# Kernel optimization log

Hardware: AMD Instinct MI355X
Metric: run time of the kernel (lower is better)

The kernel has to match this reference:

```python
import jax, jax.numpy as jnp
import numpy as np

N_NODES = 50000
N_EDGES = 500000
NFEAT = 128
NHID = 128
NOUT = 16


def setup_inputs() -> dict:
    key = jax.random.key(0)
    ks = jax.random.split(key, 8)
    x = jax.random.normal(ks[0], (N_NODES, NFEAT), dtype=jnp.float32)
    edge_src = jax.random.randint(ks[1], (N_EDGES,), 0, N_NODES, dtype=jnp.int32)
    edge_dst = jax.random.randint(ks[2], (N_EDGES,), 0, N_NODES, dtype=jnp.int32)
    edge_weight = jax.random.uniform(ks[3], (N_EDGES,), dtype=jnp.float32)
    # Glorot-ish init for linear weights, zero bias (PyG GCNConv default bias=0)
    def glorot(k, fan_in, fan_out):
        s = jnp.sqrt(6.0 / (fan_in + fan_out))
        return jax.random.uniform(k, (fan_in, fan_out), jnp.float32, -s, s)
    W1 = glorot(ks[4], NFEAT, NHID)
    W2 = glorot(ks[5], NHID, NHID)
    W3 = glorot(ks[6], NHID, NOUT)
    b1 = jnp.zeros((NHID,), jnp.float32)
    b2 = jnp.zeros((NHID,), jnp.float32)
    b3 = jnp.zeros((NOUT,), jnp.float32)
    return {"x": x, "edge_src": edge_src, "edge_dst": edge_dst,
            "edge_weight": edge_weight, "W1": W1, "b1": b1,
            "W2": W2, "b2": b2, "W3": W3, "b3": b3}


def gcn_conv(x, src, dst, ew, W, b):
    """PyG GCNConv: symmetric-normalized aggregation with self-loops (weight 1).

    out_i = sum_{(j->i)} d_i^{-1/2} w_ji d_j^{-1/2} (x_j W) + d_i^{-1} (x_i W) + b
    where d_i = 1 + sum of incoming edge weights.
    """
    n = x.shape[0]
    xw = x @ W                                            # [N, F_out]
    deg = jax.ops.segment_sum(ew, dst, num_segments=n) + 1.0  # self-loop weight 1
    dinv = jnp.where(deg > 0, jax.lax.rsqrt(deg), 0.0)    # d^{-1/2}
    norm = dinv[src] * ew * dinv[dst]                     # [E]
    agg = jax.ops.segment_sum(xw[src] * norm[:, None], dst, num_segments=n)
    self_loop = xw * (dinv * dinv)[:, None]               # d_i^{-1} * x_i W
    return agg + self_loop + b


def reference(x, edge_src, edge_dst, edge_weight, W1, b1, W2, b2, W3, b3):
    # Dropout layers are identity in eval mode.
    h = gcn_conv(x, edge_src, edge_dst, edge_weight, W1, b1)
    h = jax.nn.relu(h)
    h = gcn_conv(h, edge_src, edge_dst, edge_weight, W2, b2)
    h = jax.nn.relu(h)
    h = gcn_conv(h, edge_src, edge_dst, edge_weight, W3, b3)
    return jax.nn.log_softmax(h, axis=1)
```

## Files before the change

### kernel.cpp

```cpp
#include <hip/hip_runtime.h>
#include <math.h>

#define NN 50000
#define NE 500000
#define NF 128
#define NO 16
#define SCAN_B 1024
#define NPART 16
#define EBL 1954

static_assert(NN < 65536, "src must fit u16");

typedef _Float16 f16x8 __attribute__((ext_vector_type(8)));
typedef _Float16 f16x4 __attribute__((ext_vector_type(4)));
typedef float f32x4 __attribute__((ext_vector_type(4)));

union HU { unsigned short u; _Float16 h; };

__device__ inline float rec_w(unsigned int rec) {
    HU cu; cu.u = (unsigned short)(rec >> 16);
    return (float)cu.h;
}


__global__ void k_count_rank(const int* __restrict__ dst, int* __restrict__ pcnt,
                             int* __restrict__ rank, int E,
                             const float* __restrict__ W1, const float* __restrict__ W2,
                             _Float16* __restrict__ W1T, _Float16* __restrict__ W2T) {
    int b = blockIdx.x;
    if (b < EBL) {
        int part = b & (NPART - 1);
        int e = b * 256 + threadIdx.x;
        if (e < E) {
            int d = dst[e];
            rank[e] = atomicAdd(&pcnt[part * NN + d], 1);
        }
    } else {
        int idx = (b - EBL) * 256 + threadIdx.x;
        int r = idx >> 7, c = idx & 127;
        W1T[(size_t)c * NF + r] = (_Float16)W1[idx];
        W2T[(size_t)c * NF + r] = (_Float16)W2[idx];
    }
}

__global__ void k_scan1f(int* __restrict__ pcnt, int* __restrict__ offs_p,
                         int* __restrict__ bsums, int N) {
    __shared__ int sm[SCAN_B];
    int t = threadIdx.x;
    int i = blockIdx.x * SCAN_B + t;
    int c = 0;
    if (i < N) {
        int run = 0;
#pragma unroll
        for (int p = 0; p < NPART; ++p) {
            int v = pcnt[p * NN + i];
            pcnt[p * NN + i] = run;
            run += v;
        }
        c = run;
    }
    sm[t] = c;
    __syncthreads();
    for (int off = 1; off < SCAN_B; off <<= 1) {
        int x = (t >= off) ? sm[t - off] : 0;
        __syncthreads();
        sm[t] += x;
        __syncthreads();
    }
    if (i < N) offs_p[i] = sm[t] - c;
    if (t == SCAN_B - 1) bsums[blockIdx.x] = sm[t];
}

__global__ void k_scan2(int* __restrict__ bsums, int NB) {
    int t = threadIdx.x;
    int v = (t < NB) ? bsums[t] : 0;
    int orig = v;
#pragma unroll
    for (int off = 1; off < 64; off <<= 1) {
        int u = __shfl_up(v, off, 64);
        if (t >= off) v += u;
    }
    if (t < NB) bsums[t] = v - orig;
}

__global__ void k_scan3x(const int* __restrict__ offs_p, const int* __restrict__ bsums,
                         int* __restrict__ pcnt, int* __restrict__ offs_f, int E) {
    int i = blockIdx.x * blockDim.x + threadIdx.x;
    if (i < NPART * NN) {
        int p = i / NN;
        int n = i - p * NN;
        int v = offs_p[n] + bsums[n >> 10];
        pcnt[i] += v;
        if (p == 0) offs_f[n] = v;
    } else if (i == NPART * NN) {
        offs_f[NN] = E;
    }
}

__global__ void k_scatter(const int* __restrict__ src, const int* __restrict__ dst,
                          const float* __restrict__ ew, const int* __restrict__ pcnt,
                          const int* __restrict__ rank, unsigned int* __restrict__ erec, int E) {
    int part = blockIdx.x & (NPART - 1);
    int e = blockIdx.x * blockDim.x + threadIdx.x;
    if (e < E) {
        int d = dst[e];
        int pos = pcnt[part * NN + d] + rank[e];
        HU cu; cu.h = (_Float16)ew[e];
        erec[pos] = (unsigned int)src[e] | ((unsigned int)cu.u << 16);
    }
}

__global__ void k_dinv_csr(const unsigned int* __restrict__ erec, const int* __restrict__ offs,
                           float* __restrict__ dinv, int N) {
    int n = blockIdx.x * blockDim.x + threadIdx.x;
    if (n < N) {
        float deg = 1.0f;
        int s = offs[n], e = offs[n + 1];
        for (int j = s; j < e; ++j) deg += rec_w(erec[j]);
        dinv[n] = rsqrtf(deg);
    }
}


__device__ inline f16x8 afrag_load(const float* X, int row, int k0) {
    const float4* p = (const float4*)(X + (size_t)row * NF + k0);
    float4 a = p[0], b = p[1];
    f16x8 r;
    r[0] = (_Float16)a.x; r[1] = (_Float16)a.y; r[2] = (_Float16)a.z; r[3] = (_Float16)a.w;
    r[4] = (_Float16)b.x; r[5] = (_Float16)b.y; r[6] = (_Float16)b.z; r[7] = (_Float16)b.w;
    return r;
}
__device__ inline f16x8 afrag_load(const _Float16* X, int row, int k0) {
    return *(const f16x8*)(X + (size_t)row * NF + k0);
}

template <typename TA>
__global__ __launch_bounds__(256) void k_gemm_mfma(const TA* __restrict__ X,
                                                   const _Float16* __restrict__ WT,
                                                   const float* __restrict__ dinv,
                                                   _Float16* __restrict__ Z, int M) {
    __shared__ _Float16 ls[4][16 * 136];
    const int tid  = threadIdx.x;
    const int w    = tid >> 6;
    const int lane = tid & 63;
    const int n16  = lane & 15;
    const int quad = lane >> 4;
    const int r0   = blockIdx.x * 64 + w * 16;

    int arow = r0 + n16; if (arow > M - 1) arow = M - 1;

    f32x4 acc[8];
#pragma unroll
    for (int c = 0; c < 8; ++c) acc[c] = (f32x4){0.f, 0.f, 0.f, 0.f};

#pragma unroll
    for (int kk = 0; kk < 4; ++kk) {
        int k0 = kk * 32 + quad * 8;
        f16x8 a = afrag_load(X, arow, k0);
#pragma unroll
        for (int c = 0; c < 8; ++c) {
            f16x8 b = *(const f16x8*)(WT + (size_t)(c * 16 + n16) * NF + k0);
            acc[c] = __builtin_amdgcn_mfma_f32_16x16x32_f16(a, b, acc[c], 0, 0, 0);
        }
    }

#pragma unroll
    for (int reg = 0; reg < 4; ++reg) {
        int lrow = quad * 4 + reg;
        int grow = r0 + lrow; if (grow > M - 1) grow = M - 1;
        float di = dinv[grow];
#pragma unroll
        for (int c = 0; c < 8; ++c)
            ls[w][lrow * 136 + c * 16 + n16] = (_Float16)(acc[c][reg] * di);
    }
    __syncthreads();
#pragma unroll
    for (int i = 0; i < 4; ++i) {
        int off16 = i * 64 + lane;
        int row = off16 >> 4;
        int col = off16 & 15;
        int grow = r0 + row;
        if (grow < M) {
            f16x8 v = *(const f16x8*)(&ls[w][row * 136 + col * 8]);
            *(f16x8*)(Z + (size_t)grow * NF + col * 8) = v;
        }
    }
}

__global__ __launch_bounds__(256) void k_agg128h(const _Float16* __restrict__ z,
                                                 const float* __restrict__ dinv,
                                                 const int* __restrict__ offs,
                                                 const unsigned int* __restrict__ erec,
                                                 const float* __restrict__ bias,
                                                 _Float16* __restrict__ hout, int relu) {
    const int tid  = threadIdx.x;
    const int lane = tid & 63;
    const int half = lane >> 5;
    const int li   = lane & 31;
    int n = __builtin_amdgcn_readfirstlane(blockIdx.x * 4 + (tid >> 6));

    float acc0 = 0.f, acc1 = 0.f, acc2 = 0.f, acc3 = 0.f;

    int s = offs[n], e = offs[n + 1];
    for (int base = s; base < e; base += 64) {
        int cnt = e - base; if (cnt > 64) cnt = 64;
        unsigned int rec = 0u;
        if (lane < cnt) rec = erec[base + lane];
        int   my_s = rec & 0xFFFF;
        float my_w = rec_w(rec);
        int k = 0;
        for (; k + 7 < cnt; k += 8) {
            int e0 = k + half, e1 = k + 2 + half, e2 = k + 4 + half, e3 = k + 6 + half;
            int s0 = __shfl(my_s, e0, 64), s1 = __shfl(my_s, e1, 64);
            int s2 = __shfl(my_s, e2, 64), s3 = __shfl(my_s, e3, 64);
            float w0 = __shfl(my_w, e0, 64), w1 = __shfl(my_w, e1, 64);
            float w2 = __shfl(my_w, e2, 64), w3 = __shfl(my_w, e3, 64);
            f16x4 v0 = *(const f16x4*)(z + ((size_t)s0 << 7) + li * 4);
            f16x4 v1 = *(const f16x4*)(z + ((size_t)s1 << 7) + li * 4);
            f16x4 v2 = *(const f16x4*)(z + ((size_t)s2 << 7) + li * 4);
            f16x4 v3 = *(const f16x4*)(z + ((size_t)s3 << 7) + li * 4);
            acc0 = fmaf((float)v0[0], w0, acc0); acc1 = fmaf((float)v0[1], w0, acc1);
            acc2 = fmaf((float)v0[2], w0, acc2); acc3 = fmaf((float)v0[3], w0, acc3);
            acc0 = fmaf((float)v1[0], w1, acc0); acc1 = fmaf((float)v1[1], w1, acc1);
            acc2 = fmaf((float)v1[2], w1, acc2); acc3 = fmaf((float)v1[3], w1, acc3);
            acc0 = fmaf((float)v2[0], w2, acc0); acc1 = fmaf((float)v2[1], w2, acc1);
            acc2 = fmaf((float)v2[2], w2, acc2); acc3 = fmaf((float)v2[3], w2, acc3);
            acc0 = fmaf((float)v3[0], w3, acc0); acc1 = fmaf((float)v3[1], w3, acc1);
            acc2 = fmaf((float)v3[2], w3, acc2); acc3 = fmaf((float)v3[3], w3, acc3);
        }
        for (; k < cnt; k += 2) {
            int eidx = k + half;
            int ec = eidx < cnt ? eidx : cnt - 1;
            int   s0 = __shfl(my_s, ec, 64);
            float wt = __shfl(my_w, ec, 64);
            float w0 = (eidx < cnt) ? wt : 0.0f;
            f16x4 v0 = *(const f16x4*)(z + ((size_t)s0 << 7) + li * 4);
            acc0 = fmaf((float)v0[0], w0, acc0); acc1 = fmaf((float)v0[1], w0, acc1);
            acc2 = fmaf((float)v0[2], w0, acc2); acc3 = fmaf((float)v0[3], w0, acc3);
        }
    }
    acc0 += __shfl_xor(acc0, 32, 64);
    acc1 += __shfl_xor(acc1, 32, 64);
    acc2 += __shfl_xor(acc2, 32, 64);
    acc3 += __shfl_xor(acc3, 32, 64);

    f16x4 sv = *(const f16x4*)(z + ((size_t)n << 7) + li * 4);
    float di = dinv[n];
    float4 bb = *(const float4*)(bias + li * 4);
    float r0 = fmaf(di, (float)sv[0] + acc0, bb.x);
    float r1 = fmaf(di, (float)sv[1] + acc1, bb.y);
    float r2 = fmaf(di, (float)sv[2] + acc2, bb.z);
    float r3 = fmaf(di, (float)sv[3] + acc3, bb.w);
    if (relu) {
        r0 = fmaxf(r0, 0.0f); r1 = fmaxf(r1, 0.0f);
        r2 = fmaxf(r2, 0.0f); r3 = fmaxf(r3, 0.0f);
    }
    if (half == 0) {
        f16x4 o;
        o[0] = (_Float16)r0; o[1] = (_Float16)r1;
        o[2] = (_Float16)r2; o[3] = (_Float16)r3;
        *(f16x4*)(hout + ((size_t)n << 7) + li * 4) = o;
    }
}

__global__ __launch_bounds__(256) void k_gemm16(const _Float16* __restrict__ H,
                                                const float* __restrict__ W3,
                                                const float* __restrict__ dinv,
                                                _Float16* __restrict__ Z3, int M) {
    __shared__ float Wl[NF * NO];
    __shared__ float Hs[16 * 132];
    int tid = threadIdx.x;
    for (int i = tid; i < NF * NO; i += 256) Wl[i] = W3[i];
    int n0 = blockIdx.x * 16;
    {
        int row = tid >> 4, h8 = tid & 15;
        int gr = n0 + row; if (gr > M - 1) gr = M - 1;
        f16x8 v = *(const f16x8*)(H + (size_t)gr * NF + h8 * 8);
        float4 f0 = {(float)v[0], (float)v[1], (float)v[2], (float)v[3]};
        float4 f1 = {(float)v[4], (float)v[5], (float)v[6], (float)v[7]};
        *(float4*)(&Hs[row * 132 + h8 * 8])     = f0;
        *(float4*)(&Hs[row * 132 + h8 * 8 + 4]) = f1;
    }
    __syncthreads();
    int ln = tid >> 4, c = tid & 15;
    float acc = 0.0f;
#pragma unroll 8
    for (int k = 0; k < NF; ++k) acc = fmaf(Hs[ln * 132 + k], Wl[k * NO + c], acc);
    int n = n0 + ln;
    if (n < M) Z3[(size_t)n * NO + c] = (_Float16)(acc * dinv[n]);
}

__global__ __launch_bounds__(256) void k_agg16_ls(const _Float16* __restrict__ z3,
                                                  const float* __restrict__ dinv,
                                                  const int* __restrict__ offs,
                                                  const unsigned int* __restrict__ erec,
                                                  const float* __restrict__ bias,
                                                  float* __restrict__ out) {
    int tid = threadIdx.x;
    int ln = tid >> 4, c = tid & 15;
    int n = blockIdx.x * 16 + ln;
    float acc = (float)z3[((size_t)n << 4) + c];
    int s = offs[n], e = offs[n + 1];
    int j = s;
    for (; j + 1 < e; j += 2) {
        unsigned int r0 = erec[j], r1 = erec[j + 1];
        acc = fmaf((float)z3[((size_t)(r0 & 0xFFFF) << 4) + c], rec_w(r0), acc);
        acc = fmaf((float)z3[((size_t)(r1 & 0xFFFF) << 4) + c], rec_w(r1), acc);
    }
    if (j < e) {
        unsigned int r0 = erec[j];
        acc = fmaf((float)z3[((size_t)(r0 & 0xFFFF) << 4) + c], rec_w(r0), acc);
    }
    acc = fmaf(dinv[n], acc, bias[c]);
    float m = acc;
#pragma unroll
    for (int off = 8; off > 0; off >>= 1) m = fmaxf(m, __shfl_xor(m, off, 16));
    float ex = expf(acc - m);
    float ss = ex;
#pragma unroll
    for (int off = 8; off > 0; off >>= 1) ss += __shfl_xor(ss, off, 16);
    out[(size_t)n * NO + c] = acc - m - logf(ss);
}


extern "C" void kernel_launch(void* const* d_in, const int* in_sizes, int n_in,
                              void* d_out, int out_size, void* d_ws, size_t ws_size,
                              hipStream_t stream) {
    const float* x   = (const float*)d_in[0];
    const int*   esrc= (const int*)  d_in[1];
    const int*   edst= (const int*)  d_in[2];
    const float* ew  = (const float*)d_in[3];
    const float* W1  = (const float*)d_in[4];
    const float* b1  = (const float*)d_in[5];
    const float* W2  = (const float*)d_in[6];
    const float* b2  = (const float*)d_in[7];
    const float* W3  = (const float*)d_in[8];
    const float* b3  = (const float*)d_in[9];
    float* out = (float*)d_out;

    char* p = (char*)d_ws;
    _Float16* z   = (_Float16*)p; p += (size_t)NN * NF * 2;
    _Float16* h   = (_Float16*)p; p += (size_t)NN * NF * 2;
    _Float16* z3  = (_Float16*)p; p += (size_t)NN * NO * 2;
    float* dinv   = (float*)p; p += (size_t)NN * 4;
    unsigned int* erec = (unsigned int*)p; p += (size_t)NE * 4;
    int*   rank   = (int*)p;   p += (size_t)NE * 4;
    int*   pcnt   = (int*)p;   p += (size_t)NPART * NN * 4;
    int*   offs_p = (int*)p;   p += (size_t)(NN + 1) * 4;
    int*   offs_f = (int*)p;   p += (size_t)(NN + 1) * 4;
    int*   bsums  = (int*)p;   p += 256;
    _Float16* W1T = (_Float16*)p; p += (size_t)NF * NF * 2;
    _Float16* W2T = (_Float16*)p; p += (size_t)NF * NF * 2;

    const int NB  = (NN + SCAN_B - 1) / SCAN_B;
    const int NBL = (NN + 255) / 256;

    hipMemsetAsync(pcnt, 0, (size_t)NPART * NN * 4, stream);

    k_count_rank<<<EBL + 64, 256, 0, stream>>>(edst, pcnt, rank, NE, W1, W2, W1T, W2T);
    k_scan1f<<<NB, SCAN_B, 0, stream>>>(pcnt, offs_p, bsums, NN);
    k_scan2<<<1, 64, 0, stream>>>(bsums, NB);
    k_scan3x<<<(NPART * NN + 256) / 256, 256, 0, stream>>>(offs_p, bsums, pcnt, offs_f, NE);
    k_scatter<<<EBL, 256, 0, stream>>>(esrc, edst, ew, pcnt, rank, erec, NE);
    k_dinv_csr<<<NBL, 256, 0, stream>>>(erec, offs_f, dinv, NN);

    k_gemm_mfma<float><<<(NN + 63) / 64, 256, 0, stream>>>(x, W1T, dinv, z, NN);
    k_agg128h<<<NN / 4, 256, 0, stream>>>(z, dinv, offs_f, erec, b1, h, 1);
    k_gemm_mfma<_Float16><<<(NN + 63) / 64, 256, 0, stream>>>(h, W2T, dinv, z, NN);
    k_agg128h<<<NN / 4, 256, 0, stream>>>(z, dinv, offs_f, erec, b2, h, 1);
    k_gemm16<<<(NN + 15) / 16, 256, 0, stream>>>(h, W3, dinv, z3, NN);
    k_agg16_ls<<<NN / 16, 256, 0, stream>>>(z3, dinv, offs_f, erec, b3, out);
}
```

Measured before the change: 251.0 us.

## Fold scan fixup into scatter/dinv and split aggregation into feature slices

Removes the k_scan3x kernel: scatter and the degree kernel now compute final CSR offsets on the fly from the block-local scan plus block sums, and the degree kernel also writes offs_f. The 128-wide aggregation kernel is restructured so each block handles one 32-feature slice for 4 nodes. Each wavefront processes 8 edges at a time with 8 lanes per edge, so the grid is four times larger. This trades one launch and a pass over the partition counts for extra per-edge index and weight shuffles. It also means each edge list is re-read once per slice, in exchange for more parallelism and shorter per-node loops.

```diff
diff --git a/kernel.cpp b/kernel.cpp
--- a/kernel.cpp
+++ b/kernel.cpp
@@ -83,39 +83,31 @@
     if (t < NB) bsums[t] = v - orig;
 }
 
-__global__ void k_scan3x(const int* __restrict__ offs_p, const int* __restrict__ bsums,
-                         int* __restrict__ pcnt, int* __restrict__ offs_f, int E) {
-    int i = blockIdx.x * blockDim.x + threadIdx.x;
-    if (i < NPART * NN) {
-        int p = i / NN;
-        int n = i - p * NN;
-        int v = offs_p[n] + bsums[n >> 10];
-        pcnt[i] += v;
-        if (p == 0) offs_f[n] = v;
-    } else if (i == NPART * NN) {
-        offs_f[NN] = E;
-    }
-}
-
 __global__ void k_scatter(const int* __restrict__ src, const int* __restrict__ dst,
                           const float* __restrict__ ew, const int* __restrict__ pcnt,
-                          const int* __restrict__ rank, unsigned int* __restrict__ erec, int E) {
+                          const int* __restrict__ rank,
+                          const int* __restrict__ offs_p, const int* __restrict__ bsums,
+                          unsigned int* __restrict__ erec, int E) {
     int part = blockIdx.x & (NPART - 1);
     int e = blockIdx.x * blockDim.x + threadIdx.x;
     if (e < E) {
         int d = dst[e];
-        int pos = pcnt[part * NN + d] + rank[e];
+        int pos = offs_p[d] + bsums[d >> 10] + pcnt[part * NN + d] + rank[e];
         HU cu; cu.h = (_Float16)ew[e];
         erec[pos] = (unsigned int)src[e] | ((unsigned int)cu.u << 16);
     }
 }
 
-__global__ void k_dinv_csr(const unsigned int* __restrict__ erec, const int* __restrict__ offs,
-                           float* __restrict__ dinv, int N) {
+__global__ void k_dinv_csr(const unsigned int* __restrict__ erec,
+                           const int* __restrict__ offs_p, const int* __restrict__ bsums,
+                           int* __restrict__ offs_f, float* __restrict__ dinv, int N, int E) {
     int n = blockIdx.x * blockDim.x + threadIdx.x;
     if (n < N) {
+        int s = offs_p[n] + bsums[n >> 10];
+        int e = (n + 1 < N) ? offs_p[n + 1] + bsums[(n + 1) >> 10] : E;
+        offs_f[n] = s;
+        if (n == N - 1) offs_f[N] = E;
         float deg = 1.0f;
-        int s = offs[n], e = offs[n + 1];
         for (int j = s; j < e; ++j) deg += rec_w(erec[j]);
         dinv[n] = rsqrtf(deg);
     }
@@ -187,19 +179,22 @@
     }
 }
 
-__global__ __launch_bounds__(256) void k_agg128h(const _Float16* __restrict__ z,
+__global__ __launch_bounds__(256) void k_agg_s32(const _Float16* __restrict__ z,
                                                  const float* __restrict__ dinv,
                                                  const int* __restrict__ offs,
                                                  const unsigned int* __restrict__ erec,
                                                  const float* __restrict__ bias,
                                                  _Float16* __restrict__ hout, int relu) {
-    const int tid  = threadIdx.x;
-    const int lane = tid & 63;
-    const int half = lane >> 5;
-    const int li   = lane & 31;
-    int n = __builtin_amdgcn_readfirstlane(blockIdx.x * 4 + (tid >> 6));
-
-    float acc0 = 0.f, acc1 = 0.f, acc2 = 0.f, acc3 = 0.f;
+    const int tid   = threadIdx.x;
+    const int lane  = tid & 63;
+    const int eslot = lane >> 3;
+    const int li    = lane & 7;
+    const int slice = blockIdx.x & 3;
+    int n = __builtin_amdgcn_readfirstlane((blockIdx.x >> 2) * 4 + (tid >> 6));
+
+    const int fbase = slice * 32 + li * 4;
+
+    float a0 = 0.f, a1 = 0.f, a2 = 0.f, a3 = 0.f;
 
     int s = offs[n], e = offs[n + 1];
     for (int base = s; base < e; base += 64) {
@@ -210,56 +205,45 @@
         float my_w = rec_w(rec);
         int k = 0;
         for (; k + 7 < cnt; k += 8) {
-            int e0 = k + half, e1 = k + 2 + half, e2 = k + 4 + half, e3 = k + 6 + half;
-            int s0 = __shfl(my_s, e0, 64), s1 = __shfl(my_s, e1, 64);
-            int s2 = __shfl(my_s, e2, 64), s3 = __shfl(my_s, e3, 64);
-            float w0 = __shfl(my_w, e0, 64), w1 = __shfl(my_w, e1, 64);
-            float w2 = __shfl(my_w, e2, 64), w3 = __shfl(my_w, e3, 64);
-            f16x4 v0 = *(const f16x4*)(z + ((size_t)s0 << 7) + li * 4);
-            f16x4 v1 = *(const f16x4*)(z + ((size_t)s1 << 7) + li * 4);
-            f16x4 v2 = *(const f16x4*)(z + ((size_t)s2 << 7) + li * 4);
-            f16x4 v3 = *(const f16x4*)(z + ((size_t)s3 << 7) + li * 4);
-            acc0 = fmaf((float)v0[0], w0, acc0); acc1 = fmaf((float)v0[1], w0, acc1);
-            acc2 = fmaf((float)v0[2], w0, acc2); acc3 = fmaf((float)v0[3], w0, acc3);
-            acc0 = fmaf((float)v1[0], w1, acc0); acc1 = fmaf((float)v1[1], w1, acc1);
-            acc2 = fmaf((float)v1[2], w1, acc2); acc3 = fmaf((float)v1[3], w1, acc3);
-            acc0 = fmaf((float)v2[0], w2, acc0); acc1 = fmaf((float)v2[1], w2, acc1);
-            acc2 = fmaf((float)v2[2], w2, acc2); acc3 = fmaf((float)v2[3], w2, acc3);
-            acc0 = fmaf((float)v3[0], w3, acc0); acc1 = fmaf((float)v3[1], w3, acc1);
-            acc2 = fmaf((float)v3[2], w3, acc2); acc3 = fmaf((float)v3[3], w3, acc3);
-        }
-        for (; k < cnt; k += 2) {
-            int eidx = k + half;
-            int ec = eidx < cnt ? eidx : cnt - 1;
+            int el = k + eslot;
+            int   s0 = __shfl(my_s, el, 64);
+            float w0 = __shfl(my_w, el, 64);
+            f16x4 v = *(const f16x4*)(z + ((size_t)s0 << 7) + fbase);
+            a0 = fmaf((float)v[0], w0, a0); a1 = fmaf((float)v[1], w0, a1);
+            a2 = fmaf((float)v[2], w0, a2); a3 = fmaf((float)v[3], w0, a3);
+        }
+        if (k < cnt) {
+            int el = k + eslot;
+            int ec = el < cnt ? el : cnt - 1;
             int   s0 = __shfl(my_s, ec, 64);
             float wt = __shfl(my_w, ec, 64);
-            float w0 = (eidx < cnt) ? wt : 0.0f;
-            f16x4 v0 = *(const f16x4*)(z + ((size_t)s0 << 7) + li * 4);
-            acc0 = fmaf((float)v0[0], w0, acc0); acc1 = fmaf((float)v0[1], w0, acc1);
-            acc2 = fmaf((float)v0[2], w0, acc2); acc3 = fmaf((float)v0[3], w0, acc3);
-        }
-    }
-    acc0 += __shfl_xor(acc0, 32, 64);
-    acc1 += __shfl_xor(acc1, 32, 64);
-    acc2 += __shfl_xor(acc2, 32, 64);
-    acc3 += __shfl_xor(acc3, 32, 64);
-
-    f16x4 sv = *(const f16x4*)(z + ((size_t)n << 7) + li * 4);
+            float w0 = (el < cnt) ? wt : 0.0f;
+            f16x4 v = *(const f16x4*)(z + ((size_t)s0 << 7) + fbase);
+            a0 = fmaf((float)v[0], w0, a0); a1 = fmaf((float)v[1], w0, a1);
+            a2 = fmaf((float)v[2], w0, a2); a3 = fmaf((float)v[3], w0, a3);
+        }
+    }
+    a0 += __shfl_xor(a0, 8, 64); a0 += __shfl_xor(a0, 16, 64); a0 += __shfl_xor(a0, 32, 64);
+    a1 += __shfl_xor(a1, 8, 64); a1 += __shfl_xor(a1, 16, 64); a1 += __shfl_xor(a1, 32, 64);
+    a2 += __shfl_xor(a2, 8, 64); a2 += __shfl_xor(a2, 16, 64); a2 += __shfl_xor(a2, 32, 64);
+    a3 += __shfl_xor(a3, 8, 64); a3 += __shfl_xor(a3, 16, 64); a3 += __shfl_xor(a3, 32, 64);
+
+    f16x4 sv = *(const f16x4*)(z + ((size_t)n << 7) + fbase);
     float di = dinv[n];
-    float4 bb = *(const float4*)(bias + li * 4);
-    float r0 = fmaf(di, (float)sv[0] + acc0, bb.x);
-    float r1 = fmaf(di, (float)sv[1] + acc1, bb.y);
-    float r2 = fmaf(di, (float)sv[2] + acc2, bb.z);
-    float r3 = fmaf(di, (float)sv[3] + acc3, bb.w);
+    float4 bb = *(const float4*)(bias + fbase);
+    float r0 = fmaf(di, (float)sv[0] + a0, bb.x);
+    float r1 = fmaf(di, (float)sv[1] + a1, bb.y);
+    float r2 = fmaf(di, (float)sv[2] + a2, bb.z);
+    float r3 = fmaf(di, (float)sv[3] + a3, bb.w);
     if (relu) {
         r0 = fmaxf(r0, 0.0f); r1 = fmaxf(r1, 0.0f);
         r2 = fmaxf(r2, 0.0f); r3 = fmaxf(r3, 0.0f);
     }
-    if (half == 0) {
+    if (eslot == 0) {
         f16x4 o;
         o[0] = (_Float16)r0; o[1] = (_Float16)r1;
         o[2] = (_Float16)r2; o[3] = (_Float16)r3;
-        *(f16x4*)(hout + ((size_t)n << 7) + li * 4) = o;
+        *(f16x4*)(hout + ((size_t)n << 7) + fbase) = o;
     }
 }
 
@@ -360,14 +344,14 @@
     k_count_rank<<<EBL + 64, 256, 0, stream>>>(edst, pcnt, rank, NE, W1, W2, W1T, W2T);
     k_scan1f<<<NB, SCAN_B, 0, stream>>>(pcnt, offs_p, bsums, NN);
     k_scan2<<<1, 64, 0, stream>>>(bsums, NB);
-    k_scan3x<<<(NPART * NN + 256) / 256, 256, 0, stream>>>(offs_p, bsums, pcnt, offs_f, NE);
-    k_scatter<<<EBL, 256, 0, stream>>>(esrc, edst, ew, pcnt, rank, erec, NE);
-    k_dinv_csr<<<NBL, 256, 0, stream>>>(erec, offs_f, dinv, NN);
-
+    k_scatter<<<EBL, 256, 0, stream>>>(esrc, edst, ew, pcnt, rank, offs_p, bsums, erec, NE);
+    k_dinv_csr<<<NBL, 256, 0, stream>>>(erec, offs_p, bsums, offs_f, dinv, NN, NE);
+
+    const int AGG_GRID = (NN / 4) * 4;
     k_gemm_mfma<float><<<(NN + 63) / 64, 256, 0, stream>>>(x, W1T, dinv, z, NN);
-    k_agg128h<<<NN / 4, 256, 0, stream>>>(z, dinv, offs_f, erec, b1, h, 1);
+    k_agg_s32<<<AGG_GRID, 256, 0, stream>>>(z, dinv, offs_f, erec, b1, h, 1);
     k_gemm_mfma<_Float16><<<(NN + 63) / 64, 256, 0, stream>>>(h, W2T, dinv, z, NN);
-    k_agg128h<<<NN / 4, 256, 0, stream>>>(z, dinv, offs_f, erec, b2, h, 1);
+    k_agg_s32<<<AGG_GRID, 256, 0, stream>>>(z, dinv, offs_f, erec, b2, h, 1);
     k_gemm16<<<(NN + 15) / 16, 256, 0, stream>>>(h, W3, dinv, z3, NN);
     k_agg16_ls<<<NN / 16, 256, 0, stream>>>(z3, dinv, offs_f, erec, b3, out);
 }
```

New measurement: 309.9 us. 1.23x slower.

## Fuse CSR scan stages and degree computation, cutting preprocessing kernel launches

Applied to the files above, without the earlier changes.

Degree is now accumulated with float atomics during the counting pass, and dinv is computed inside the first scan kernel. A last-block-done pattern folds the block-sum scan into that same kernel. The offset-fixup and dinv kernels are removed, and consumers rebuild row offsets from offs_p plus bsums on the fly. This drops three kernel launches and one full pass over pcnt. In exchange it adds per-edge float atomics, an extra partition buffer to zero in the memset, and nontemporal hints on the aggregation loads and stores.

```diff
diff --git a/kernel.cpp b/kernel.cpp
--- a/kernel.cpp
+++ b/kernel.cpp
@@ -6,6 +6,7 @@
 #define NF 128
 #define NO 16
 #define SCAN_B 1024
+#define NB_SCAN 49
 #define NPART 16
 #define EBL 1954
 
@@ -23,7 +24,8 @@
 }
 
 
-__global__ void k_count_rank(const int* __restrict__ dst, int* __restrict__ pcnt,
+__global__ void k_count_rank(const int* __restrict__ dst, const float* __restrict__ ew,
+                             int* __restrict__ pcnt, float* __restrict__ pdeg,
                              int* __restrict__ rank, int E,
                              const float* __restrict__ W1, const float* __restrict__ W2,
                              _Float16* __restrict__ W1T, _Float16* __restrict__ W2T) {
@@ -34,6 +36,7 @@
         if (e < E) {
             int d = dst[e];
             rank[e] = atomicAdd(&pcnt[part * NN + d], 1);
+            atomicAdd(&pdeg[part * NN + d], ew[e]);
         }
     } else {
         int idx = (b - EBL) * 256 + threadIdx.x;
@@ -43,13 +46,15 @@
     }
 }
 
-__global__ void k_scan1f(int* __restrict__ pcnt, int* __restrict__ offs_p,
-                         int* __restrict__ bsums, int N) {
+__global__ void k_scan1f(int* __restrict__ pcnt, const float* __restrict__ pdeg,
+                         int* __restrict__ offs_p, int* __restrict__ bsums,
+                         float* __restrict__ dinv, int* __restrict__ done) {
     __shared__ int sm[SCAN_B];
+    __shared__ int isLast;
     int t = threadIdx.x;
     int i = blockIdx.x * SCAN_B + t;
     int c = 0;
-    if (i < N) {
+    if (i < NN) {
         int run = 0;
 #pragma unroll
         for (int p = 0; p < NPART; ++p) {
@@ -58,6 +63,10 @@
             run += v;
         }
         c = run;
+        float deg = 1.0f;
+#pragma unroll
+        for (int p = 0; p < NPART; ++p) deg += pdeg[p * NN + i];
+        dinv[i] = rsqrtf(deg);
     }
     sm[t] = c;
     __syncthreads();
@@ -67,57 +76,42 @@
         sm[t] += x;
         __syncthreads();
     }
-    if (i < N) offs_p[i] = sm[t] - c;
-    if (t == SCAN_B - 1) bsums[blockIdx.x] = sm[t];
-}
-
-__global__ void k_scan2(int* __restrict__ bsums, int NB) {
-    int t = threadIdx.x;
-    int v = (t < NB) ? bsums[t] : 0;
-    int orig = v;
-#pragma unroll
-    for (int off = 1; off < 64; off <<= 1) {
-        int u = __shfl_up(v, off, 64);
-        if (t >= off) v += u;
-    }
-    if (t < NB) bsums[t] = v - orig;
-}
-
-__global__ void k_scan3x(const int* __restrict__ offs_p, const int* __restrict__ bsums,
-                         int* __restrict__ pcnt, int* __restrict__ offs_f, int E) {
-    int i = blockIdx.x * blockDim.x + threadIdx.x;
-    if (i < NPART * NN) {
-        int p = i / NN;
-        int n = i - p * NN;
-        int v = offs_p[n] + bsums[n >> 10];
-        pcnt[i] += v;
-        if (p == 0) offs_f[n] = v;
-    } else if (i == NPART * NN) {
-        offs_f[NN] = E;
+    if (i < NN) offs_p[i] = sm[t] - c;
+    if (t == SCAN_B - 1) {
+        __hip_atomic_store(&bsums[blockIdx.x], sm[t], __ATOMIC_RELEASE,
+                           __HIP_MEMORY_SCOPE_AGENT);
+        int old = __hip_atomic_fetch_add(done, 1, __ATOMIC_ACQ_REL,
+                                         __HIP_MEMORY_SCOPE_AGENT);
+        isLast = (old == (int)gridDim.x - 1) ? 1 : 0;
+    }
+    __syncthreads();
+    if (isLast && t < 64) {
+        int v = (t < NB_SCAN) ? __hip_atomic_load(&bsums[t], __ATOMIC_ACQUIRE,
+                                                  __HIP_MEMORY_SCOPE_AGENT) : 0;
+        int orig = v;
+#pragma unroll
+        for (int off = 1; off < 64; off <<= 1) {
+            int u = __shfl_up(v, off, 64);
+            if (t >= off) v += u;
+        }
+        if (t < NB_SCAN)
+            __hip_atomic_store(&bsums[t], v - orig, __ATOMIC_RELEASE,
+                               __HIP_MEMORY_SCOPE_AGENT);
     }
 }
 
 __global__ void k_scatter(const int* __restrict__ src, const int* __restrict__ dst,
                           const float* __restrict__ ew, const int* __restrict__ pcnt,
-                          const int* __restrict__ rank, unsigned int* __restrict__ erec, int E) {
+                          const int* __restrict__ rank,
+                          const int* __restrict__ offs_p, const int* __restrict__ bsums,
+                          unsigned int* __restrict__ erec, int E) {
     int part = blockIdx.x & (NPART - 1);
     int e = blockIdx.x * blockDim.x + threadIdx.x;
     if (e < E) {
         int d = dst[e];
-        int pos = pcnt[part * NN + d] + rank[e];
+        int pos = offs_p[d] + bsums[d >> 10] + pcnt[part * NN + d] + rank[e];
         HU cu; cu.h = (_Float16)ew[e];
         erec[pos] = (unsigned int)src[e] | ((unsigned int)cu.u << 16);
-    }
-}
-
-__global__ void k_dinv_csr(const unsigned int* __restrict__ erec, const int* __restrict__ offs,
-                           float* __restrict__ dinv, int N) {
-    int n = blockIdx.x * blockDim.x + threadIdx.x;
-    if (n < N) {
-        float deg = 1.0f;
-        int s = offs[n], e = offs[n + 1];
-        for (int j = s; j < e; ++j) deg += rec_w(erec[j]);
-        dinv[n] = rsqrtf(deg);
     }
 }
 
@@ -189,7 +183,8 @@
 
 __global__ __launch_bounds__(256) void k_agg128h(const _Float16* __restrict__ z,
                                                  const float* __restrict__ dinv,
-                                                 const int* __restrict__ offs,
+                                                 const int* __restrict__ offs_p,
+                                                 const int* __restrict__ bsums,
                                                  const unsigned int* __restrict__ erec,
                                                  const float* __restrict__ bias,
                                                  _Float16* __restrict__ hout, int relu) {
@@ -201,11 +196,12 @@
 
     float acc0 = 0.f, acc1 = 0.f, acc2 = 0.f, acc3 = 0.f;
 
-    int s = offs[n], e = offs[n + 1];
+    int s = offs_p[n] + bsums[n >> 10];
+    int e = (n + 1 < NN) ? offs_p[n + 1] + bsums[(n + 1) >> 10] : NE;
     for (int base = s; base < e; base += 64) {
         int cnt = e - base; if (cnt > 64) cnt = 64;
         unsigned int rec = 0u;
-        if (lane < cnt) rec = erec[base + lane];
+        if (lane < cnt) rec = __builtin_nontemporal_load(erec + base + lane);
         int   my_s = rec & 0xFFFF;
         float my_w = rec_w(rec);
         int k = 0;
@@ -259,7 +255,7 @@
         f16x4 o;
         o[0] = (_Float16)r0; o[1] = (_Float16)r1;
         o[2] = (_Float16)r2; o[3] = (_Float16)r3;
-        *(f16x4*)(hout + ((size_t)n << 7) + li * 4) = o;
+        __builtin_nontemporal_store(o, (f16x4*)(hout + ((size_t)n << 7) + li * 4));
     }
 }
 
@@ -292,7 +288,8 @@
 
 __global__ __launch_bounds__(256) void k_agg16_ls(const _Float16* __restrict__ z3,
                                                   const float* __restrict__ dinv,
-                                                  const int* __restrict__ offs,
+                                                  const int* __restrict__ offs_p,
+                                                  const int* __restrict__ bsums,
                                                   const unsigned int* __restrict__ erec,
                                                   const float* __restrict__ bias,
                                                   float* __restrict__ out) {
@@ -300,7 +297,8 @@
     int ln = tid >> 4, c = tid & 15;
     int n = blockIdx.x * 16 + ln;
     float acc = (float)z3[((size_t)n << 4) + c];
-    int s = offs[n], e = offs[n + 1];
+    int s = offs_p[n] + bsums[n >> 10];
+    int e = (n + 1 < NN) ? offs_p[n + 1] + bsums[(n + 1) >> 10] : NE;
     int j = s;
     for (; j + 1 < e; j += 2) {
         unsigned int r0 = erec[j], r1 = erec[j + 1];
@@ -346,28 +344,24 @@
     unsigned int* erec = (unsigned int*)p; p += (size_t)NE * 4;
     int*   rank   = (int*)p;   p += (size_t)NE * 4;
     int*   pcnt   = (int*)p;   p += (size_t)NPART * NN * 4;
+    float* pdeg   = (float*)p; p += (size_t)NPART * NN * 4;
+    int*   done   = (int*)p;   p += 64;
     int*   offs_p = (int*)p;   p += (size_t)(NN + 1) * 4;
-    int*   offs_f = (int*)p;   p += (size_t)(NN + 1) * 4;
     int*   bsums  = (int*)p;   p += 256;
     _Float16* W1T = (_Float16*)p; p += (size_t)NF * NF * 2;
     _Float16* W2T = (_Float16*)p; p += (size_t)NF * NF * 2;
 
-    const int NB  = (NN + SCAN_B - 1) / SCAN_B;
-    const int NBL = (NN + 255) / 256;
-
-    hipMemsetAsync(pcnt, 0, (size_t)NPART * NN * 4, stream);
-
-    k_count_rank<<<EBL + 64, 256, 0, stream>>>(edst, pcnt, rank, NE, W1, W2, W1T, W2T);
-    k_scan1f<<<NB, SCAN_B, 0, stream>>>(pcnt, offs_p, bsums, NN);
-    k_scan2<<<1, 64, 0, stream>>>(bsums, NB);
-    k_scan3x<<<(NPART * NN + 256) / 256, 256, 0, stream>>>(offs_p, bsums, pcnt, offs_f, NE);
-    k_scatter<<<EBL, 256, 0, stream>>>(esrc, edst, ew, pcnt, rank, erec, NE);
-    k_dinv_csr<<<NBL, 256, 0, stream>>>(erec, offs_f, dinv, NN);
+    hipMemsetAsync(pcnt, 0, (size_t)NPART * NN * 4 * 2 + 64, stream);
+
+    k_count_rank<<<EBL + 64, 256, 0, stream>>>(edst, ew, pcnt, pdeg, rank, NE,
+                                               W1, W2, W1T, W2T);
+    k_scan1f<<<NB_SCAN, SCAN_B, 0, stream>>>(pcnt, pdeg, offs_p, bsums, dinv, done);
+    k_scatter<<<EBL, 256, 0, stream>>>(esrc, edst, ew, pcnt, rank, offs_p, bsums, erec, NE);
 
     k_gemm_mfma<float><<<(NN + 63) / 64, 256, 0, stream>>>(x, W1T, dinv, z, NN);
-    k_agg128h<<<NN / 4, 256, 0, stream>>>(z, dinv, offs_f, erec, b1, h, 1);
+    k_agg128h<<<NN / 4, 256, 0, stream>>>(z, dinv, offs_p, bsums, erec, b1, h, 1);
     k_gemm_mfma<_Float16><<<(NN + 63) / 64, 256, 0, stream>>>(h, W2T, dinv, z, NN);
-    k_agg128h<<<NN / 4, 256, 0, stream>>>(z, dinv, offs_f, erec, b2, h, 1);
+    k_agg128h<<<NN / 4, 256, 0, stream>>>(z, dinv, offs_p, bsums, erec, b2, h, 1);
     k_gemm16<<<(NN + 15) / 16, 256, 0, stream>>>(h, W3, dinv, z3, NN);
-    k_agg16_ls<<<NN / 16, 256, 0, stream>>>(z3, dinv, offs_f, erec, b3, out);
-}
+    k_agg16_ls<<<NN / 16, 256, 0, stream>>>(z3, dinv, offs_p, bsums, erec, b3, out);
+}
```

New measurement: 273.3 us. 8.9% more time.
